# Optimization experiments

Measured on AMD Instinct MI355X. Metric: run time of the kernel, lower is better.

The kernel has to match this reference:

```python
import jax, jax.numpy as jnp
import numpy as np

INVALID_CLS = tuple(range(240, 256))
TEMPERATURE = 1.0
PRED_PER_IM = 100
B, Q, C = 256, 900, 256


def setup_inputs() -> dict:
    key = jax.random.key(0)
    k1, k2, k3, k4 = jax.random.split(key, 4)
    pred_logits = jax.random.normal(k1, (B, Q, C), dtype=jnp.float32)
    pred_obj = jax.random.uniform(k2, (B, Q), dtype=jnp.float32)
    pred_boxes = jax.random.uniform(k3, (B, Q, 4), dtype=jnp.float32)
    # target sizes ~ realistic image resolutions (h, w)
    target_sizes = jax.random.uniform(k4, (B, 2), dtype=jnp.float32) * 800.0 + 200.0
    return {"pred_logits": pred_logits, "pred_obj": pred_obj,
            "pred_boxes": pred_boxes, "target_sizes": target_sizes}


def _cxcywh_to_xyxy(boxes):
    cx, cy, w, h = jnp.split(boxes, 4, axis=-1)
    return jnp.concatenate([cx - 0.5 * w, cy - 0.5 * h,
                            cx + 0.5 * w, cy + 0.5 * h], axis=-1)


def reference(pred_logits, pred_obj, pred_boxes, target_sizes):
    b, q, c = pred_logits.shape
    invalid = jnp.array(INVALID_CLS)
    logits = pred_logits.at[:, :, invalid].set(-1e11)
    # fused probability: exp(-T * energy) * sigmoid(logits)
    obj_prob = jnp.exp(-TEMPERATURE * pred_obj)[..., None]          # [B,Q,1]
    fused = obj_prob * jax.nn.sigmoid(logits)                       # [B,Q,C]
    scores, topk_idx = jax.lax.top_k(fused.reshape(b, q * c), PRED_PER_IM)
    topk_boxes = topk_idx // c                                      # [B,K]
    labels = topk_idx % c                                           # [B,K]
    boxes_xyxy = _cxcywh_to_xyxy(pred_boxes)                        # [B,Q,4]
    gather_idx = jnp.broadcast_to(topk_boxes[:, :, None], (b, PRED_PER_IM, 4))
    boxes = jnp.take_along_axis(boxes_xyxy, gather_idx, axis=1)     # [B,K,4]
    img_h, img_w = target_sizes[:, 0], target_sizes[:, 1]
    scale = jnp.stack([img_w, img_h, img_w, img_h], axis=1)         # [B,4]
    boxes = boxes * scale[:, None, :]
    return scores, labels, boxes
```

## Files before the change

### kernel.cpp

```cpp
#include <hip/hip_runtime.h>
#include <stdint.h>

#define NB 256
#define NQ 900
#define NC 256
#define TOPK 100
#define QC (NQ * NC)
#define NBINS_S 4096
#define CAP 4096
#define FCAP 512
#define KS 25
#define SHIFT 18


__device__ __forceinline__ float fastsig(float x) {
    return __builtin_amdgcn_rcpf(1.0f + __expf(-x));
}

__global__ __launch_bounds__(1024)
void postproc_kernel(const float* __restrict__ logits,
                     const float* __restrict__ obj,
                     const float* __restrict__ pboxes,
                     const float* __restrict__ tsz,
                     float* __restrict__ out)
{
    const int b = blockIdx.x;
    const int tid = threadIdx.x;
    const int wid = tid >> 6;
    const int lane = tid & 63;

    __shared__ unsigned int pool[NBINS_S];
    __shared__ float eobj[NQ];
    __shared__ float xthrRow[NQ];
    __shared__ unsigned int cbits[CAP];
    __shared__ int cidx[CAP];
    __shared__ int activeQ[NQ];
    __shared__ unsigned int part[1024];
    __shared__ unsigned int part2[32];
    __shared__ int s_thrBin, s_cnt, s_nActive, s_c2;
    __shared__ int s_cut, s_dig, s_above, s_nfin;

    unsigned int* shist = pool;

    for (int i = tid; i < NBINS_S; i += 1024) shist[i] = 0;
    if (tid == 0) { s_cnt = 0; s_nActive = 0; }
    if (tid < NQ) eobj[tid] = expf(-obj[b * NQ + tid]);
    __syncthreads();

    const float4* lg4 = (const float4*)(logits + (size_t)b * QC);

    for (int j = wid; j < 56; j += 16) {
        int q = j * 16 + 8;
        if (lane < 60) {
            float eo = eobj[q];
            float4 v = lg4[(q << 6) + lane];
            atomicAdd(&shist[__float_as_uint(eo * fastsig(v.x)) >> SHIFT], 1u);
            atomicAdd(&shist[__float_as_uint(eo * fastsig(v.y)) >> SHIFT], 1u);
            atomicAdd(&shist[__float_as_uint(eo * fastsig(v.z)) >> SHIFT], 1u);
            atomicAdd(&shist[__float_as_uint(eo * fastsig(v.w)) >> SHIFT], 1u);
        }
    }
    __syncthreads();

    {
        unsigned int sum = 0;
        #pragma unroll
        for (int j = 0; j < 4; ++j) sum += shist[tid * 4 + j];
        part[tid] = sum;
    }
    __syncthreads();
    if (tid < 32) {
        unsigned int s2 = 0;
        #pragma unroll
        for (int j = 0; j < 32; ++j) s2 += part[tid * 32 + j];
        part2[tid] = s2;
    }
    __syncthreads();
    if (tid == 0) {
        int cum = 0;
        int sc = 31;
        while (sc > 0 && cum + (int)part2[sc] < KS) { cum += (int)part2[sc]; --sc; }
        int pc = sc * 32 + 31, plo = sc * 32;
        while (pc > plo && cum + (int)part[pc] < KS) { cum += (int)part[pc]; --pc; }
        int bin = pc * 4 + 3, blo = pc * 4;
        while (bin > blo && cum + (int)shist[bin] < KS) { cum += (int)shist[bin]; --bin; }
        s_thrBin = bin;
    }
    __syncthreads();
    unsigned int thrBits = (unsigned int)s_thrBin << SHIFT;
    const float thrF = __uint_as_float(thrBits);

    const unsigned rangeSel = 0x3F800000u - thrBits;
    int FS = 0;
    if ((int)rangeSel >= 4096) { int hb = 31 - __builtin_clz(rangeSel); FS = hb - 11; }

    if (tid < NQ) {
        if (__float_as_uint(eobj[tid]) >= thrBits) {
            int p = atomicAdd(&s_nActive, 1);
            activeQ[p] = tid;
            float t = thrF / eobj[tid];
            float r = t / (1.0f - t);
            xthrRow[tid] = logf(r) - 0.01f;
        }
    }
    for (int i = tid; i < NBINS_S; i += 1024) pool[i] = 0;
    __syncthreads();
    const int nA = s_nActive;

    for (int j = wid; j < nA; j += 16) {
        int q = activeQ[j];
        float xt = xthrRow[q];
        if (lane < 60) {
            float4 v = lg4[(q << 6) + lane];
            #pragma unroll
            for (int j2 = 0; j2 < 4; ++j2) {
                float x = (j2 == 0) ? v.x : (j2 == 1) ? v.y : (j2 == 2) ? v.z : v.w;
                if (x >= xt) {
                    int p = atomicAdd(&s_cnt, 1);
                    if (p < CAP) {
                        cbits[p] = __float_as_uint(x);
                        cidx[p] = (q << 8) + (lane << 2) + j2;
                    }
                }
            }
        }
    }
    __syncthreads();
    const int npreRaw = s_cnt;
    const int npre = min(npreRaw, CAP);

    int myN = 0;
    int midx0 = 0, midx1 = 0, midx2 = 0, midx3 = 0;
    float mlog0 = 0.f, mlog1 = 0.f, mlog2 = 0.f, mlog3 = 0.f;
    {
        int i = tid;
        if (i < npre) { midx0 = cidx[i]; mlog0 = __uint_as_float(cbits[i]); myN = 1; i += 1024; }
        if (i < npre) { midx1 = cidx[i]; mlog1 = __uint_as_float(cbits[i]); myN = 2; i += 1024; }
        if (i < npre) { midx2 = cidx[i]; mlog2 = __uint_as_float(cbits[i]); myN = 3; i += 1024; }
        if (i < npre) { midx3 = cidx[i]; mlog3 = __uint_as_float(cbits[i]); myN = 4; }
    }
    __syncthreads();
    if (tid == 0) s_cnt = 0;
    __syncthreads();

    #pragma unroll
    for (int k = 0; k < 4; ++k) {
        if (k < myN) {
            float x  = (k == 0) ? mlog0 : (k == 1) ? mlog1 : (k == 2) ? mlog2 : mlog3;
            int  idx = (k == 0) ? midx0 : (k == 1) ? midx1 : (k == 2) ? midx2 : midx3;
            float eo = eobj[idx >> 8];
            float s = eo * (1.0f / (1.0f + expf(-x)));
            unsigned bits = __float_as_uint(s);
            if (bits >= thrBits) {
                int p = atomicAdd(&s_cnt, 1);
                if (p < CAP) {
                    cbits[p] = bits;
                    cidx[p] = idx;
                    atomicAdd(&pool[(bits - thrBits) >> FS], 1u);
                }
            }
        }
    }
    __syncthreads();
    int M = s_cnt;
    const bool fbUsed = (M < TOPK || npreRaw > CAP);

    if (fbUsed) {
        int lo = 0, hi = NBINS_S - 1;
        while (lo < hi) {
            int mid = (lo + hi + 1) >> 1;
            unsigned int tb = (unsigned int)mid << SHIFT;
            if (tid == 0) s_c2 = 0;
            __syncthreads();
            int local = 0;
            for (int j = wid; j < NQ; j += 16) {
                if (__float_as_uint(eobj[j]) >= tb && lane < 60) {
                    float eo = eobj[j];
                    float4 v = lg4[(j << 6) + lane];
                    local += (__float_as_uint(eo * (1.0f / (1.0f + expf(-v.x)))) >= tb);
                    local += (__float_as_uint(eo * (1.0f / (1.0f + expf(-v.y)))) >= tb);
                    local += (__float_as_uint(eo * (1.0f / (1.0f + expf(-v.z)))) >= tb);
                    local += (__float_as_uint(eo * (1.0f / (1.0f + expf(-v.w)))) >= tb);
                }
            }
            atomicAdd(&s_c2, local);
            __syncthreads();
            if (s_c2 >= TOPK) lo = mid; else hi = mid - 1;
            __syncthreads();
        }
        unsigned int tb = (unsigned int)lo << SHIFT;
        thrBits = tb;
        if (tid == 0) s_cnt = 0;
        __syncthreads();
        for (int j = wid; j < NQ; j += 16) {
            if (__float_as_uint(eobj[j]) >= tb && lane < 60) {
                float eo = eobj[j];
                float4 v = lg4[(j << 6) + lane];
                #pragma unroll
                for (int j2 = 0; j2 < 4; ++j2) {
                    float x = (j2 == 0) ? v.x : (j2 == 1) ? v.y : (j2 == 2) ? v.z : v.w;
                    float s = eo * (1.0f / (1.0f + expf(-x)));
                    unsigned int bits = __float_as_uint(s);
                    if (bits >= tb) {
                        int p = atomicAdd(&s_cnt, 1);
                        if (p < CAP) {
                            cbits[p] = bits;
                            cidx[p] = (j << 8) + (lane << 2) + j2;
                        }
                    }
                }
            }
        }
        __syncthreads();
        M = s_cnt;
    }
    M = min(M, CAP);

    unsigned selBits = 0;
    bool haveSel = false;

    if (!fbUsed) {
        {
            unsigned int sum = 0;
            #pragma unroll
            for (int j = 0; j < 4; ++j) sum += pool[tid * 4 + j];
            part[tid] = sum;
        }
        __syncthreads();
        if (tid < 32) {
            unsigned int s2 = 0;
            #pragma unroll
            for (int j = 0; j < 32; ++j) s2 += part[tid * 32 + j];
            part2[tid] = s2;
        }
        __syncthreads();
        if (tid == 0) {
            int cum = 0;
            int sc = 31;
            while (sc > 0 && cum + (int)part2[sc] < TOPK) { cum += (int)part2[sc]; --sc; }
            int pc = sc * 32 + 31, plo = sc * 32;
            while (pc > plo && cum + (int)part[pc] < TOPK) { cum += (int)part[pc]; --pc; }
            int bin = pc * 4 + 3, blo = pc * 4;
            while (bin > blo && cum + (int)pool[bin] < TOPK) { cum += (int)pool[bin]; --bin; }
            s_cut = bin;
        }
        __syncthreads();
        selBits = thrBits + ((unsigned)s_cut << FS);
        haveSel = true;

        unsigned int* fb = pool;
        int* fi = (int*)(pool + FCAP);
        if (tid == 0) s_nfin = 0;
        __syncthreads();
        for (int i = tid; i < M; i += 1024) {
            unsigned int bb = cbits[i];
            if (bb >= selBits) {
                int p = atomicAdd(&s_nfin, 1);
                if (p < FCAP) { fb[p] = bb; fi[p] = cidx[i]; }
            }
        }
        __syncthreads();
        if (s_nfin > FCAP) haveSel = false;
    }

    if (!haveSel) {
        unsigned int* rhist = part;
        unsigned int* rsuf  = part + 256;
        unsigned int prefixVal = 0;
        int need = TOPK;
        int startShift = 24;
        if ((thrBits >> 24) == 0x3Fu) { prefixVal = 0x3F000000u; startShift = 16; }
        for (int shift = startShift; shift >= 0; shift -= 8) {
            if (tid < 256) rhist[tid] = 0;
            __syncthreads();
            unsigned int pmask = (shift >= 24) ? 0u : (0xFFFFFFFFu << (shift + 8));
            for (int i = tid; i < M; i += 1024) {
                unsigned int bb = cbits[i];
                if ((bb & pmask) == (prefixVal & pmask))
                    atomicAdd(&rhist[(bb >> shift) & 255], 1u);
            }
            __syncthreads();
            if (tid < 64) {
                unsigned int h0 = rhist[tid * 4 + 0];
                unsigned int h1 = rhist[tid * 4 + 1];
                unsigned int h2 = rhist[tid * 4 + 2];
                unsigned int h3 = rhist[tid * 4 + 3];
                unsigned int loc = h0 + h1 + h2 + h3;
                unsigned int suf = loc;
                #pragma unroll
                for (int d = 1; d < 64; d <<= 1) {
                    unsigned int o = __shfl_down(suf, d);
                    suf += (tid + d < 64) ? o : 0u;
                }
                unsigned int above = suf - loc;
                rsuf[tid * 4 + 3] = above + h3;
                rsuf[tid * 4 + 2] = above + h3 + h2;
                rsuf[tid * 4 + 1] = above + h3 + h2 + h1;
                rsuf[tid * 4 + 0] = above + h3 + h2 + h1 + h0;
            }
            __syncthreads();
            if (tid < 256) {
                int sv = (int)rsuf[tid];
                int sa = (tid == 255) ? 0 : (int)rsuf[tid + 1];
                if (sv >= need && sa < need) { s_dig = tid; s_above = sa; }
            }
            __syncthreads();
            prefixVal |= ((unsigned int)s_dig) << shift;
            need -= s_above;
        }
        selBits = prefixVal;

        unsigned int* fb = pool;
        int* fi = (int*)(pool + FCAP);
        if (tid == 0) s_nfin = 0;
        __syncthreads();
        for (int i = tid; i < M; i += 1024) {
            unsigned int bb = cbits[i];
            if (bb >= selBits) {
                int p = atomicAdd(&s_nfin, 1);
                if (p < FCAP) { fb[p] = bb; fi[p] = cidx[i]; }
            }
        }
        __syncthreads();
    }
    const int n = min(s_nfin, FCAP);

    unsigned int* fb = pool;
    int* fi = (int*)(pool + FCAP);
    const float ih = tsz[b * 2 + 0];
    const float iw = tsz[b * 2 + 1];
    float* out_scores = out;
    float* out_labels = out + NB * TOPK;
    float* out_boxes  = out + 2 * NB * TOPK;

    for (int i = tid; i < n; i += 1024) {
        unsigned int mb = fb[i];
        int mi = fi[i];
        int rank = 0;
        for (int j = 0; j < n; ++j) {
            unsigned int ob = fb[j];
            int oi = fi[j];
            rank += (ob > mb) || (ob == mb && oi < mi);
        }
        if (rank < TOPK) {
            int q = mi >> 8;
            int c = mi & 255;
            out_scores[b * TOPK + rank] = __uint_as_float(mb);
            out_labels[b * TOPK + rank] = (float)c;
            const float* bp = pboxes + ((size_t)b * NQ + q) * 4;
            float cx = bp[0], cy = bp[1], w = bp[2], h = bp[3];
            float* dst = out_boxes + ((size_t)b * TOPK + rank) * 4;
            dst[0] = (cx - 0.5f * w) * iw;
            dst[1] = (cy - 0.5f * h) * ih;
            dst[2] = (cx + 0.5f * w) * iw;
            dst[3] = (cy + 0.5f * h) * ih;
        }
    }
}

extern "C" void kernel_launch(void* const* d_in, const int* in_sizes, int n_in,
                              void* d_out, int out_size, void* d_ws, size_t ws_size,
                              hipStream_t stream) {
    const float* logits = (const float*)d_in[0];
    const float* obj    = (const float*)d_in[1];
    const float* boxes  = (const float*)d_in[2];
    const float* tsz    = (const float*)d_in[3];
    float* out = (float*)d_out;
    hipLaunchKernelGGL(postproc_kernel, dim3(NB), dim3(1024), 0, stream,
                       logits, obj, boxes, tsz, out);
}
```

Baseline: 32.40 us.

## Prefetch sample rows and likely-active logit rows into registers before histogram passes

```diff
diff --git a/kernel.cpp b/kernel.cpp
--- a/kernel.cpp
+++ b/kernel.cpp
@@ -11,13 +11,15 @@
 #define FCAP 512
 #define KS 25
 #define SHIFT 18
+#define RT 272
+#define RLCAP 288
 
 
 __device__ __forceinline__ float fastsig(float x) {
     return __builtin_amdgcn_rcpf(1.0f + __expf(-x));
 }
 
-__global__ __launch_bounds__(1024)
+__global__ __launch_bounds__(1024, 1)
 void postproc_kernel(const float* __restrict__ logits,
                      const float* __restrict__ obj,
                      const float* __restrict__ pboxes,
@@ -34,38 +36,100 @@
     __shared__ float xthrRow[NQ];
     __shared__ unsigned int cbits[CAP];
     __shared__ int cidx[CAP];
-    __shared__ int activeQ[NQ];
+    __shared__ unsigned short remQ[NQ];
+    __shared__ unsigned short rowlist[RLCAP];
+    __shared__ unsigned char rowPref[NQ];
     __shared__ unsigned int part[1024];
     __shared__ unsigned int part2[32];
-    __shared__ int s_thrBin, s_cnt, s_nActive, s_c2;
+    __shared__ int s_bin, s_cnt, s_nrl, s_nrem, s_c2;
     __shared__ int s_cut, s_dig, s_above, s_nfin;
 
-    unsigned int* shist = pool;
-
-    for (int i = tid; i < NBINS_S; i += 1024) shist[i] = 0;
-    if (tid == 0) { s_cnt = 0; s_nActive = 0; }
-    if (tid < NQ) eobj[tid] = expf(-obj[b * NQ + tid]);
-    __syncthreads();
-
     const float4* lg4 = (const float4*)(logits + (size_t)b * QC);
 
-    for (int j = wid; j < 56; j += 16) {
-        int q = j * 16 + 8;
-        if (lane < 60) {
-            float eo = eobj[q];
-            float4 v = lg4[(q << 6) + lane];
-            atomicAdd(&shist[__float_as_uint(eo * fastsig(v.x)) >> SHIFT], 1u);
-            atomicAdd(&shist[__float_as_uint(eo * fastsig(v.y)) >> SHIFT], 1u);
-            atomicAdd(&shist[__float_as_uint(eo * fastsig(v.z)) >> SHIFT], 1u);
-            atomicAdd(&shist[__float_as_uint(eo * fastsig(v.w)) >> SHIFT], 1u);
-        }
+    float4 smp[4];
+    #pragma unroll
+    for (int r = 0; r < 4; ++r) {
+        int j = wid + 16 * r;
+        if (j < 56) smp[r] = lg4[((j * 16 + 8) << 6) + lane];
+    }
+
+    for (int i = tid; i < NBINS_S; i += 1024) pool[i] = 0;
+    if (tid == 0) { s_cnt = 0; s_nrl = 0; s_nrem = 0; }
+    if (tid < NQ) { eobj[tid] = expf(-obj[b * NQ + tid]); rowPref[tid] = 0; }
+    __syncthreads();
+
+    if (tid < NQ) {
+        unsigned eb = __float_as_uint(eobj[tid]);
+        int bin = (int)(eb >> 15) - 0x7D00;
+        bin = min(4095, max(0, bin));
+        atomicAdd(&pool[bin], 1u);
     }
     __syncthreads();
 
     {
         unsigned int sum = 0;
         #pragma unroll
-        for (int j = 0; j < 4; ++j) sum += shist[tid * 4 + j];
+        for (int j = 0; j < 4; ++j) sum += pool[tid * 4 + j];
+        part[tid] = sum;
+    }
+    __syncthreads();
+    if (tid < 32) {
+        unsigned int s2 = 0;
+        #pragma unroll
+        for (int j = 0; j < 32; ++j) s2 += part[tid * 32 + j];
+        part2[tid] = s2;
+    }
+    __syncthreads();
+    if (tid == 0) {
+        int cum = 0;
+        int sc = 31;
+        while (sc > 0 && cum + (int)part2[sc] < RT) { cum += (int)part2[sc]; --sc; }
+        int pc = sc * 32 + 31, plo = sc * 32;
+        while (pc > plo && cum + (int)part[pc] < RT) { cum += (int)part[pc]; --pc; }
+        int bin = pc * 4 + 3, blo = pc * 4;
+        while (bin > blo && cum + (int)pool[bin] < RT) { cum += (int)pool[bin]; --bin; }
+        s_bin = bin;
+    }
+    __syncthreads();
+    const unsigned rowEdge = ((unsigned)(s_bin + 0x7D00)) << 15;
+
+    if (tid < NQ && __float_as_uint(eobj[tid]) >= rowEdge) {
+        int p = atomicAdd(&s_nrl, 1);
+        if (p < RLCAP) { rowlist[p] = (unsigned short)tid; rowPref[tid] = 1; }
+    }
+    for (int i = tid; i < NBINS_S; i += 1024) pool[i] = 0;
+    __syncthreads();
+    const int nrl = min(s_nrl, RLCAP);
+
+    float4 pre[18];
+    #pragma unroll
+    for (int r = 0; r < 18; ++r) {
+        int idx = wid + 16 * r;
+        if (idx < nrl) {
+            int q = rowlist[idx];
+            pre[r] = lg4[(q << 6) + lane];
+        }
+    }
+
+    #pragma unroll
+    for (int r = 0; r < 4; ++r) {
+        int j = wid + 16 * r;
+        if (j < 56 && lane < 60) {
+            int q = j * 16 + 8;
+            float eo = eobj[q];
+            float4 v = smp[r];
+            atomicAdd(&pool[__float_as_uint(eo * fastsig(v.x)) >> SHIFT], 1u);
+            atomicAdd(&pool[__float_as_uint(eo * fastsig(v.y)) >> SHIFT], 1u);
+            atomicAdd(&pool[__float_as_uint(eo * fastsig(v.z)) >> SHIFT], 1u);
+            atomicAdd(&pool[__float_as_uint(eo * fastsig(v.w)) >> SHIFT], 1u);
+        }
+    }
+    __syncthreads();
+
+    {
+        unsigned int sum = 0;
+        #pragma unroll
+        for (int j = 0; j < 4; ++j) sum += pool[tid * 4 + j];
         part[tid] = sum;
     }
     __syncthreads();
@@ -83,43 +147,69 @@
         int pc = sc * 32 + 31, plo = sc * 32;
         while (pc > plo && cum + (int)part[pc] < KS) { cum += (int)part[pc]; --pc; }
         int bin = pc * 4 + 3, blo = pc * 4;
-        while (bin > blo && cum + (int)shist[bin] < KS) { cum += (int)shist[bin]; --bin; }
-        s_thrBin = bin;
-    }
-    __syncthreads();
-    unsigned int thrBits = (unsigned int)s_thrBin << SHIFT;
+        while (bin > blo && cum + (int)pool[bin] < KS) { cum += (int)pool[bin]; --bin; }
+        s_bin = bin;
+    }
+    __syncthreads();
+    unsigned int thrBits = (unsigned int)s_bin << SHIFT;
     const float thrF = __uint_as_float(thrBits);
 
     const unsigned rangeSel = 0x3F800000u - thrBits;
     int FS = 0;
     if ((int)rangeSel >= 4096) { int hb = 31 - __builtin_clz(rangeSel); FS = hb - 11; }
 
-    if (tid < NQ) {
-        if (__float_as_uint(eobj[tid]) >= thrBits) {
-            int p = atomicAdd(&s_nActive, 1);
-            activeQ[p] = tid;
-            float t = thrF / eobj[tid];
-            float r = t / (1.0f - t);
-            xthrRow[tid] = logf(r) - 0.01f;
+    if (tid < NQ && __float_as_uint(eobj[tid]) >= thrBits) {
+        float t = thrF / eobj[tid];
+        float r = t / (1.0f - t);
+        xthrRow[tid] = logf(r) - 0.01f;
+        if (!rowPref[tid]) {
+            int p = atomicAdd(&s_nrem, 1);
+            remQ[p] = (unsigned short)tid;
         }
     }
     for (int i = tid; i < NBINS_S; i += 1024) pool[i] = 0;
     __syncthreads();
-    const int nA = s_nActive;
-
-    for (int j = wid; j < nA; j += 16) {
-        int q = activeQ[j];
-        float xt = xthrRow[q];
-        if (lane < 60) {
-            float4 v = lg4[(q << 6) + lane];
-            #pragma unroll
-            for (int j2 = 0; j2 < 4; ++j2) {
-                float x = (j2 == 0) ? v.x : (j2 == 1) ? v.y : (j2 == 2) ? v.z : v.w;
-                if (x >= xt) {
-                    int p = atomicAdd(&s_cnt, 1);
-                    if (p < CAP) {
-                        cbits[p] = __float_as_uint(x);
-                        cidx[p] = (q << 8) + (lane << 2) + j2;
+
+    #pragma unroll
+    for (int r = 0; r < 18; ++r) {
+        int idx = wid + 16 * r;
+        if (idx < nrl) {
+            int q = rowlist[idx];
+            if (__float_as_uint(eobj[q]) >= thrBits) {
+                float xt = xthrRow[q];
+                if (lane < 60) {
+                    float4 v = pre[r];
+                    #pragma unroll
+                    for (int j2 = 0; j2 < 4; ++j2) {
+                        float x = (j2 == 0) ? v.x : (j2 == 1) ? v.y : (j2 == 2) ? v.z : v.w;
+                        if (x >= xt) {
+                            int p = atomicAdd(&s_cnt, 1);
+                            if (p < CAP) {
+                                cbits[p] = __float_as_uint(x);
+                                cidx[p] = (q << 8) + (lane << 2) + j2;
+                            }
+                        }
+                    }
+                }
+            }
+        }
+    }
+    {
+        const int nrem = s_nrem;
+        for (int j = wid; j < nrem; j += 16) {
+            int q = remQ[j];
+            float xt = xthrRow[q];
+            if (lane < 60) {
+                float4 v = lg4[(q << 6) + lane];
+                #pragma unroll
+                for (int j2 = 0; j2 < 4; ++j2) {
+                    float x = (j2 == 0) ? v.x : (j2 == 1) ? v.y : (j2 == 2) ? v.z : v.w;
+                    if (x >= xt) {
+                        int p = atomicAdd(&s_cnt, 1);
+                        if (p < CAP) {
+                            cbits[p] = __float_as_uint(x);
+                            cidx[p] = (q << 8) + (lane << 2) + j2;
+                        }
                     }
                 }
             }
```

Result: slower. 40.85 us (+26.1%).
